# Kernel optimization log

Measured on AMD Instinct MI355X. Metric: run time of the kernel, lower is better.

Reference implementation:

```python
import jax, jax.numpy as jnp
import numpy as np

N_NODES = 50000


def gcn_conv(x, W, b, src, dst, n):
    """PyG-style GCNConv: out = D^-1/2 (A+I) D^-1/2 (x W) + b.
    src/dst: [E] int edge endpoints (messages flow src -> dst)."""
    h = x @ W  # [n, out]
    # degree with self-loops (edge weight 1)
    deg = jax.ops.segment_sum(jnp.ones_like(dst, dtype=h.dtype), dst, num_segments=n) + 1.0
    inv_sqrt = jax.lax.rsqrt(deg)  # [n]
    coef = inv_sqrt[src] * inv_sqrt[dst]  # [E]
    msg = h[src] * coef[:, None]  # [E, out]
    agg = jax.ops.segment_sum(msg, dst, num_segments=n)
    # self-loop contribution: norm = 1/deg
    agg = agg + h * (inv_sqrt * inv_sqrt)[:, None]
    return agg + b


def encoder(x, src, dst, W_a, b_a, W_b, b_b, n):
    h = jax.nn.relu(gcn_conv(x, W_a, b_a, src, dst, n))
    return jax.nn.relu(gcn_conv(h, W_b, b_b, src, dst, n))


def setup_inputs() -> dict:
    key = jax.random.key(0)
    ks = jax.random.split(key, 8)
    N, E = N_NODES, 400000
    d_in, d_hid, d_out = 512, 512, 256
    x = jax.random.normal(ks[0], (N, d_in), dtype=jnp.float32)
    edge_index = jax.random.randint(ks[1], (2, E), 0, N, dtype=jnp.int32)
    edge_index2 = jax.random.randint(ks[2], (2, E), 0, N, dtype=jnp.int32)

    def xavier(k, shape):
        lim = np.sqrt(6.0 / (shape[0] + shape[1]))
        return jax.random.uniform(k, shape, jnp.float32, -lim, lim)

    W1 = xavier(ks[3], (d_in, d_hid))
    b1 = jnp.zeros((d_hid,), jnp.float32)
    W2 = xavier(ks[4], (d_hid, d_out))
    b2 = jnp.zeros((d_out,), jnp.float32)
    W3 = xavier(ks[5], (d_out, d_hid))
    b3 = jnp.zeros((d_hid,), jnp.float32)
    W4 = xavier(ks[6], (d_hid, d_out))
    b4 = jnp.zeros((d_out,), jnp.float32)
    return {"x": x, "edge_index": edge_index, "edge_index2": edge_index2,
            "W1": W1, "b1": b1, "W2": W2, "b2": b2,
            "W3": W3, "b3": b3, "W4": W4, "b4": b4}


def reference(x, edge_index, edge_index2, W1, b1, W2, b2, W3, b3, W4, b4):
    n = x.shape[0]
    z = encoder(x, edge_index[0], edge_index[1], W1, b1, W2, b2, n)
    z_g = encoder(z, edge_index2[0], edge_index2[1], W3, b3, W4, b4, n)
    return (z, z_g)
```

## Files before the change

kernel.cpp:

```cpp
#include <hip/hip_runtime.h>

#define N_NODES 50000
#define MP 50048

typedef short short8 __attribute__((ext_vector_type(8)));
typedef float floatx4 __attribute__((ext_vector_type(4)));
typedef ushort u16x4 __attribute__((ext_vector_type(4)));
typedef float f32x4 __attribute__((ext_vector_type(4)));

__device__ __forceinline__ float bf2f(ushort u) {
    union { unsigned int i; float f; } x; x.i = ((unsigned int)u) << 16; return x.f;
}
__device__ __forceinline__ ushort f2bf(float f) {
    union { float f; unsigned int i; } x; x.f = f;
    unsigned int r = x.i + 0x7FFFu + ((x.i >> 16) & 1u);
    return (ushort)(r >> 16);
}

__global__ __launch_bounds__(256) void deg_int_kernel(const int* __restrict__ dst,
                                                      int* __restrict__ deg, int E) {
    int i = blockIdx.x * 256 + threadIdx.x;
    if (i < E) atomicAdd(&deg[dst[i]], 1);
}
__global__ __launch_bounds__(256) void inv_from_deg(const int* __restrict__ deg,
                                                    float* __restrict__ inv, int n) {
    int i = blockIdx.x * 256 + threadIdx.x;
    if (i < n) inv[i] = rsqrtf((float)deg[i] + 1.0f);
}

__global__ __launch_bounds__(256) void scan1_kernel(const int* __restrict__ deg,
                                                    int* __restrict__ pre,
                                                    int* __restrict__ bsum, int n) {
    __shared__ int tmp[256];
    const int t = threadIdx.x;
    const int i = blockIdx.x * 256 + t;
    const int v = (i < n) ? deg[i] : 0;
    tmp[t] = v;
    __syncthreads();
#pragma unroll
    for (int d = 1; d < 256; d <<= 1) {
        int u = (t >= d) ? tmp[t - d] : 0;
        __syncthreads();
        tmp[t] += u;
        __syncthreads();
    }
    if (i < n) pre[i] = tmp[t] - v;
    if (t == 255) bsum[blockIdx.x] = tmp[255];
}
__global__ __launch_bounds__(256) void scan2_kernel(int* __restrict__ bsum, int nb,
                                                    int* __restrict__ row_ptr_n) {
    __shared__ int tmp[256];
    const int t = threadIdx.x;
    const int v = (t < nb) ? bsum[t] : 0;
    tmp[t] = v;
    __syncthreads();
#pragma unroll
    for (int d = 1; d < 256; d <<= 1) {
        int u = (t >= d) ? tmp[t - d] : 0;
        __syncthreads();
        tmp[t] += u;
        __syncthreads();
    }
    if (t < nb) bsum[t] = tmp[t] - v;
    if (t == 255) *row_ptr_n = tmp[255];
}
__global__ __launch_bounds__(256) void scan3_kernel(const int* __restrict__ pre,
                                                    const int* __restrict__ bsum,
                                                    int* __restrict__ row_ptr,
                                                    int* __restrict__ cursor, int n) {
    const int i = blockIdx.x * 256 + threadIdx.x;
    if (i < n) {
        int v = pre[i] + bsum[blockIdx.x];
        row_ptr[i] = v;
        cursor[i] = v;
    }
}
__global__ __launch_bounds__(256) void fill_adj_kernel(const int* __restrict__ src,
                                                       const int* __restrict__ dst,
                                                       const float* __restrict__ invs,
                                                       int* __restrict__ cursor,
                                                       int* __restrict__ adj,
                                                       float* __restrict__ wgt, int E) {
    int i = blockIdx.x * 256 + threadIdx.x;
    if (i < E) {
        int s = src[i];
        int pos = atomicAdd(&cursor[dst[i]], 1);
        adj[pos] = s;
        wgt[pos] = invs[s];
    }
}

__global__ __launch_bounds__(256) void f2b_kernel(const float* __restrict__ in,
                                                  ushort* __restrict__ out, int n) {
    int i = blockIdx.x * 256 + threadIdx.x;
    if (i < n) out[i] = f2bf(in[i]);
}
__global__ __launch_bounds__(256) void transpose_kernel(const float* __restrict__ W,
                                                        ushort* __restrict__ Wt, int K, int N) {
    int idx = blockIdx.x * 256 + threadIdx.x;
    if (idx < K * N) {
        int k = idx / N, n = idx % N;
        Wt[n * K + k] = f2bf(W[idx]);
    }
}

__global__ __launch_bounds__(512, 4) void gemm_kernel(
    const ushort* __restrict__ A, const ushort* __restrict__ Bt,
    ushort* __restrict__ C, const float* __restrict__ bias,
    int M, int K, int N, int do_relu)
{
    __shared__ __align__(16) ushort Alds[128 * 32];
    __shared__ __align__(16) ushort Blds[128 * 32];
    const int t = threadIdx.x;
    const int w = t >> 6, l = t & 63;
    const int m0 = blockIdx.y * 128;
    const int n0 = blockIdx.x * 128;
    const int wr = (w >> 2) * 64, wc = (w & 3) * 32;
    const int lhi = l >> 4, llo = l & 15;

    floatx4 acc[4][2] = {};

    const int srow = w * 16 + (l >> 2);
    const int scol = (l & 3) * 8;
    int gr = m0 + srow; gr = gr < M ? gr : M - 1;
    const ushort* gA = A + (size_t)gr * K + scol;
    const ushort* gB = Bt + (size_t)(n0 + srow) * K + scol;
    ushort* lA = Alds + srow * 32 + scol;
    ushort* lB = Blds + srow * 32 + scol;

    const int nkt = K >> 5;
    for (int kt = 0; kt < nkt; ++kt) {
        const int k0 = kt << 5;
        __builtin_amdgcn_global_load_lds(
            (const __attribute__((address_space(1))) void*)(gA + k0),
            (__attribute__((address_space(3))) void*)lA, 16, 0, 0);
        __builtin_amdgcn_global_load_lds(
            (const __attribute__((address_space(1))) void*)(gB + k0),
            (__attribute__((address_space(3))) void*)lB, 16, 0, 0);
        __syncthreads();
        short8 av[4], bv[2];
#pragma unroll
        for (int m = 0; m < 4; ++m)
            av[m] = *reinterpret_cast<const short8*>(&Alds[(wr + m * 16 + llo) * 32 + lhi * 8]);
#pragma unroll
        for (int n = 0; n < 2; ++n)
            bv[n] = *reinterpret_cast<const short8*>(&Blds[(wc + n * 16 + llo) * 32 + lhi * 8]);
#pragma unroll
        for (int m = 0; m < 4; ++m)
#pragma unroll
            for (int n = 0; n < 2; ++n)
                acc[m][n] = __builtin_amdgcn_mfma_f32_16x16x32_bf16(av[m], bv[n], acc[m][n], 0, 0, 0);
        __syncthreads();
    }

    const int lr = lhi * 4;
#pragma unroll
    for (int m = 0; m < 4; ++m) {
#pragma unroll
        for (int n = 0; n < 2; ++n) {
            int gcol = n0 + wc + n * 16 + llo;
            float badd = bias ? bias[gcol] : 0.0f;
#pragma unroll
            for (int j = 0; j < 4; ++j) {
                int grow = m0 + wr + m * 16 + lr + j;
                if (grow < M) {
                    float v = acc[m][n][j] + badd;
                    if (do_relu) v = fmaxf(v, 0.0f);
                    C[(size_t)grow * N + gcol] = f2bf(v);
                }
            }
        }
    }
}

template<bool RELU, bool BIAS, bool WF, bool WB>
__global__ __launch_bounds__(256) void gather_kernel(
    const int* __restrict__ row_ptr, const int* __restrict__ adj,
    const float* __restrict__ wgt,
    const ushort* __restrict__ h, int ldh,
    const float* __restrict__ invs, const float* __restrict__ bias,
    float* __restrict__ outF, ushort* __restrict__ outB, int ldo)
{
    const int wv = threadIdx.x >> 6, l = threadIdx.x & 63;
    const int node = blockIdx.x * 4 + wv;
    if (node >= N_NODES) return;
    const int c0 = blockIdx.y * 256 + l * 4;
    const int beg = row_ptr[node], end = row_ptr[node + 1];
    const float invd = invs[node];

    float a0[4] = {0.f, 0.f, 0.f, 0.f}, a1[4] = {0.f, 0.f, 0.f, 0.f};
    int e = beg;
    for (; e + 2 <= end; e += 2) {
        const int s0 = adj[e], s1 = adj[e + 1];
        const float w0 = wgt[e] * invd, w1 = wgt[e + 1] * invd;
        const u16x4 h0 = *reinterpret_cast<const u16x4*>(h + (size_t)s0 * ldh + c0);
        const u16x4 h1 = *reinterpret_cast<const u16x4*>(h + (size_t)s1 * ldh + c0);
#pragma unroll
        for (int k = 0; k < 4; ++k) {
            a0[k] += bf2f(h0[k]) * w0;
            a1[k] += bf2f(h1[k]) * w1;
        }
    }
    if (e < end) {
        const int s0 = adj[e];
        const float w0 = wgt[e] * invd;
        const u16x4 h0 = *reinterpret_cast<const u16x4*>(h + (size_t)s0 * ldh + c0);
#pragma unroll
        for (int k = 0; k < 4; ++k) a0[k] += bf2f(h0[k]) * w0;
    }
    {
        const float ws = invd * invd;
        const u16x4 hs = *reinterpret_cast<const u16x4*>(h + (size_t)node * ldh + c0);
#pragma unroll
        for (int k = 0; k < 4; ++k) a0[k] += a1[k] + bf2f(hs[k]) * ws;
    }
#pragma unroll
    for (int k = 0; k < 4; ++k) {
        float v = a0[k];
        if (BIAS) v += bias[c0 + k];
        if (RELU) v = fmaxf(v, 0.0f);
        a0[k] = v;
    }
    if (WF)
        *reinterpret_cast<f32x4*>(outF + (size_t)node * ldo + c0) = *reinterpret_cast<f32x4*>(a0);
    if (WB) {
        u16x4 o;
#pragma unroll
        for (int k = 0; k < 4; ++k) o[k] = f2bf(a0[k]);
        *reinterpret_cast<u16x4*>(outB + (size_t)node * ldo + c0) = o;
    }
}

extern "C" void kernel_launch(void* const* d_in, const int* in_sizes, int n_in,
                              void* d_out, int out_size, void* d_ws, size_t ws_size,
                              hipStream_t stream)
{
    const float* x  = (const float*)d_in[0];
    const int* ei1  = (const int*)d_in[1];
    const int* ei2  = (const int*)d_in[2];
    const float* W1 = (const float*)d_in[3];
    const float* b1 = (const float*)d_in[4];
    const float* W2 = (const float*)d_in[5];
    const float* b2 = (const float*)d_in[6];
    const float* W3 = (const float*)d_in[7];
    const float* b3 = (const float*)d_in[8];
    const float* W4 = (const float*)d_in[9];
    const float* b4 = (const float*)d_in[10];
    float* z   = (float*)d_out;
    float* z_g = z + (size_t)N_NODES * 256;

    const int E1 = in_sizes[1] / 2, E2 = in_sizes[2] / 2;
    const int* src1 = ei1;  const int* dst1 = ei1 + E1;
    const int* src2 = ei2;  const int* dst2 = ei2 + E2;

    ushort* Xb = (ushort*)z;
    ushort* R1 = (ushort*)z_g;

    char* ws = (char*)d_ws;
    size_t off = 0;
    auto alloc = [&](size_t bytes) { void* p = ws + off; off += (bytes + 255) & ~(size_t)255; return p; };
    ushort* R0   = (ushort*)alloc((size_t)N_NODES * 512 * 2);
    float*  inv1 = (float*) alloc((size_t)N_NODES * 4);
    float*  inv2 = (float*) alloc((size_t)N_NODES * 4);
    int*    deg1 = (int*)   alloc((size_t)N_NODES * 4);
    int*    deg2 = (int*)   alloc((size_t)N_NODES * 4);
    int*    rp1  = (int*)   alloc((size_t)(N_NODES + 1) * 4);
    int*    rp2  = (int*)   alloc((size_t)(N_NODES + 1) * 4);
    int*    cur1 = (int*)   alloc((size_t)N_NODES * 4);
    int*    cur2 = (int*)   alloc((size_t)N_NODES * 4);
    int*    pre1 = (int*)   alloc((size_t)N_NODES * 4);
    int*    pre2 = (int*)   alloc((size_t)N_NODES * 4);
    int*    bs1  = (int*)   alloc(256 * 4);
    int*    bs2  = (int*)   alloc(256 * 4);
    int*    adj1 = (int*)   alloc((size_t)E1 * 4);
    int*    adj2 = (int*)   alloc((size_t)E2 * 4);
    float*  wgt1 = (float*) alloc((size_t)E1 * 4);
    float*  wgt2 = (float*) alloc((size_t)E2 * 4);
    ushort* Wt1  = (ushort*)alloc(512 * 512 * 2);
    ushort* Wt2  = (ushort*)alloc(256 * 512 * 2);
    ushort* Wt3  = (ushort*)alloc(512 * 256 * 2);
    ushort* Wt4  = (ushort*)alloc(256 * 512 * 2);

    const dim3 blk(256);
    const dim3 gblk(512);
    const int MT = MP / 128;
    const int GB = (N_NODES + 3) / 4;
    const int NB = (N_NODES + 255) / 256;

    hipMemsetAsync(deg1, 0, (size_t)N_NODES * 4, stream);
    hipMemsetAsync(deg2, 0, (size_t)N_NODES * 4, stream);
    deg_int_kernel<<<(E1 + 255) / 256, blk, 0, stream>>>(dst1, deg1, E1);
    deg_int_kernel<<<(E2 + 255) / 256, blk, 0, stream>>>(dst2, deg2, E2);
    inv_from_deg<<<(N_NODES + 255) / 256, blk, 0, stream>>>(deg1, inv1, N_NODES);
    inv_from_deg<<<(N_NODES + 255) / 256, blk, 0, stream>>>(deg2, inv2, N_NODES);
    scan1_kernel<<<NB, blk, 0, stream>>>(deg1, pre1, bs1, N_NODES);
    scan1_kernel<<<NB, blk, 0, stream>>>(deg2, pre2, bs2, N_NODES);
    scan2_kernel<<<1, blk, 0, stream>>>(bs1, NB, rp1 + N_NODES);
    scan2_kernel<<<1, blk, 0, stream>>>(bs2, NB, rp2 + N_NODES);
    scan3_kernel<<<NB, blk, 0, stream>>>(pre1, bs1, rp1, cur1, N_NODES);
    scan3_kernel<<<NB, blk, 0, stream>>>(pre2, bs2, rp2, cur2, N_NODES);
    fill_adj_kernel<<<(E1 + 255) / 256, blk, 0, stream>>>(src1, dst1, inv1, cur1, adj1, wgt1, E1);
    fill_adj_kernel<<<(E2 + 255) / 256, blk, 0, stream>>>(src2, dst2, inv2, cur2, adj2, wgt2, E2);

    transpose_kernel<<<(512 * 512 + 255) / 256, blk, 0, stream>>>(W1, Wt1, 512, 512);
    transpose_kernel<<<(512 * 256 + 255) / 256, blk, 0, stream>>>(W2, Wt2, 512, 256);
    transpose_kernel<<<(256 * 512 + 255) / 256, blk, 0, stream>>>(W3, Wt3, 256, 512);
    transpose_kernel<<<(512 * 256 + 255) / 256, blk, 0, stream>>>(W4, Wt4, 512, 256);
    f2b_kernel<<<(N_NODES * 512 + 255) / 256, blk, 0, stream>>>(x, Xb, N_NODES * 512);

    gemm_kernel<<<dim3(4, MT), gblk, 0, stream>>>(Xb, Wt1, R0, nullptr, N_NODES, 512, 512, 0);
    gather_kernel<true, true, false, true><<<dim3(GB, 2), blk, 0, stream>>>(
        rp1, adj1, wgt1, R0, 512, inv1, b1, nullptr, R1, 512);

    gemm_kernel<<<dim3(2, MT), gblk, 0, stream>>>(R1, Wt2, R0, nullptr, N_NODES, 512, 256, 0);
    gather_kernel<true, true, true, true><<<dim3(GB, 1), blk, 0, stream>>>(
        rp1, adj1, wgt1, R0, 256, inv1, b2, z, R1, 256);

    gather_kernel<false, false, false, true><<<dim3(GB, 1), blk, 0, stream>>>(
        rp2, adj2, wgt2, R1, 256, inv2, nullptr, nullptr, R0, 256);
    gemm_kernel<<<dim3(4, MT), gblk, 0, stream>>>(R0, Wt3, R1, b3, N_NODES, 256, 512, 1);

    gemm_kernel<<<dim3(2, MT), gblk, 0, stream>>>(R1, Wt4, R0, nullptr, N_NODES, 512, 256, 0);
    gather_kernel<true, true, true, false><<<dim3(GB, 1), blk, 0, stream>>>(
        rp2, adj2, wgt2, R0, 256, inv2, b4, z_g, nullptr, 256);
}
```

Baseline: 513.6 us.

## Pack adjacency and weights, gather 16-byte rows with two nodes per wavefront

Stores each edge's source index and source normalization weight together as one int2, so each edge needs a single 8-byte load instead of two separate loads. The gather kernel now gives half a wavefront (32 lanes) to each node and has each lane load 8 bf16 values (16 bytes) instead of 4. The edge loop is unrolled by 4 with clamped indices and zero weights for padding edges. This is meant to cut per-edge index traffic and raise memory-level parallelism, at the cost of wasted loads when the two nodes sharing a wavefront have different degrees.

```diff
diff --git a/kernel.cpp b/kernel.cpp
--- a/kernel.cpp
+++ b/kernel.cpp
@@ -5,7 +5,7 @@
 
 typedef short short8 __attribute__((ext_vector_type(8)));
 typedef float floatx4 __attribute__((ext_vector_type(4)));
-typedef ushort u16x4 __attribute__((ext_vector_type(4)));
+typedef ushort u16x8 __attribute__((ext_vector_type(8)));
 typedef float f32x4 __attribute__((ext_vector_type(4)));
 
 __device__ __forceinline__ float bf2f(ushort u) {
@@ -79,14 +79,12 @@
                                                        const int* __restrict__ dst,
                                                        const float* __restrict__ invs,
                                                        int* __restrict__ cursor,
-                                                       int* __restrict__ adj,
-                                                       float* __restrict__ wgt, int E) {
+                                                       int2* __restrict__ adjw, int E) {
     int i = blockIdx.x * 256 + threadIdx.x;
     if (i < E) {
         int s = src[i];
         int pos = atomicAdd(&cursor[dst[i]], 1);
-        adj[pos] = s;
-        wgt[pos] = invs[s];
+        adjw[pos] = make_int2(s, __float_as_int(invs[s]));
     }
 }
 
@@ -175,59 +173,67 @@
 
 template<bool RELU, bool BIAS, bool WF, bool WB>
 __global__ __launch_bounds__(256) void gather_kernel(
-    const int* __restrict__ row_ptr, const int* __restrict__ adj,
-    const float* __restrict__ wgt,
+    const int* __restrict__ row_ptr, const int2* __restrict__ adjw,
     const ushort* __restrict__ h, int ldh,
     const float* __restrict__ invs, const float* __restrict__ bias,
     float* __restrict__ outF, ushort* __restrict__ outB, int ldo)
 {
     const int wv = threadIdx.x >> 6, l = threadIdx.x & 63;
-    const int node = blockIdx.x * 4 + wv;
-    if (node >= N_NODES) return;
-    const int c0 = blockIdx.y * 256 + l * 4;
-    const int beg = row_ptr[node], end = row_ptr[node + 1];
-    const float invd = invs[node];
-
-    float a0[4] = {0.f, 0.f, 0.f, 0.f}, a1[4] = {0.f, 0.f, 0.f, 0.f};
-    int e = beg;
-    for (; e + 2 <= end; e += 2) {
-        const int s0 = adj[e], s1 = adj[e + 1];
-        const float w0 = wgt[e] * invd, w1 = wgt[e + 1] * invd;
-        const u16x4 h0 = *reinterpret_cast<const u16x4*>(h + (size_t)s0 * ldh + c0);
-        const u16x4 h1 = *reinterpret_cast<const u16x4*>(h + (size_t)s1 * ldh + c0);
-#pragma unroll
-        for (int k = 0; k < 4; ++k) {
-            a0[k] += bf2f(h0[k]) * w0;
-            a1[k] += bf2f(h1[k]) * w1;
+    const int half = l >> 5, j = l & 31;
+    const int node = blockIdx.x * 8 + wv * 2 + half;
+    const bool valid = node < N_NODES;
+    const int nd = valid ? node : N_NODES - 1;
+    const int c0 = blockIdx.y * 256 + j * 8;
+    const int beg = row_ptr[nd], end = row_ptr[nd + 1];
+    const float invd = invs[nd];
+    const int deg = end - beg;
+    const int dmax = max(deg, __shfl_xor(deg, 32));
+
+    float a0[8] = {}, a1[8] = {};
+    const int iters = (dmax + 3) >> 2;
+    for (int it = 0; it < iters; ++it) {
+        const int e = beg + it * 4;
+#pragma unroll
+        for (int u = 0; u < 4; ++u) {
+            int ee = e + u;
+            int ec = min(ee, end - 1); ec = max(ec, 0);
+            const int2 aw = adjw[ec];
+            const float w = (ee < end) ? __int_as_float(aw.y) * invd : 0.0f;
+            const u16x8 hv = *reinterpret_cast<const u16x8*>(h + (unsigned)(aw.x * ldh + c0));
+            if (u & 1) {
+#pragma unroll
+                for (int k = 0; k < 8; ++k) a1[k] += bf2f(hv[k]) * w;
+            } else {
+#pragma unroll
+                for (int k = 0; k < 8; ++k) a0[k] += bf2f(hv[k]) * w;
+            }
         }
-    }
-    if (e < end) {
-        const int s0 = adj[e];
-        const float w0 = wgt[e] * invd;
-        const u16x4 h0 = *reinterpret_cast<const u16x4*>(h + (size_t)s0 * ldh + c0);
-#pragma unroll
-        for (int k = 0; k < 4; ++k) a0[k] += bf2f(h0[k]) * w0;
     }
     {
         const float ws = invd * invd;
-        const u16x4 hs = *reinterpret_cast<const u16x4*>(h + (size_t)node * ldh + c0);
-#pragma unroll
-        for (int k = 0; k < 4; ++k) a0[k] += a1[k] + bf2f(hs[k]) * ws;
-    }
-#pragma unroll
-    for (int k = 0; k < 4; ++k) {
+        const u16x8 hs = *reinterpret_cast<const u16x8*>(h + (unsigned)(nd * ldh + c0));
+#pragma unroll
+        for (int k = 0; k < 8; ++k) a0[k] += a1[k] + bf2f(hs[k]) * ws;
+    }
+#pragma unroll
+    for (int k = 0; k < 8; ++k) {
         float v = a0[k];
         if (BIAS) v += bias[c0 + k];
         if (RELU) v = fmaxf(v, 0.0f);
         a0[k] = v;
     }
-    if (WF)
-        *reinterpret_cast<f32x4*>(outF + (size_t)node * ldo + c0) = *reinterpret_cast<f32x4*>(a0);
-    if (WB) {
-        u16x4 o;
-#pragma unroll
-        for (int k = 0; k < 4; ++k) o[k] = f2bf(a0[k]);
-        *reinterpret_cast<u16x4*>(outB + (size_t)node * ldo + c0) = o;
+    if (valid) {
+        if (WF) {
+            float* op = outF + (size_t)node * ldo + c0;
+            *reinterpret_cast<f32x4*>(op)     = *reinterpret_cast<f32x4*>(&a0[0]);
+            *reinterpret_cast<f32x4*>(op + 4) = *reinterpret_cast<f32x4*>(&a0[4]);
+        }
+        if (WB) {
+            u16x8 o;
+#pragma unroll
+            for (int k = 0; k < 8; ++k) o[k] = f2bf(a0[k]);
+            *reinterpret_cast<u16x8*>(outB + (size_t)node * ldo + c0) = o;
+        }
     }
 }
 
@@ -272,10 +278,8 @@
     int*    pre2 = (int*)   alloc((size_t)N_NODES * 4);
     int*    bs1  = (int*)   alloc(256 * 4);
     int*    bs2  = (int*)   alloc(256 * 4);
-    int*    adj1 = (int*)   alloc((size_t)E1 * 4);
-    int*    adj2 = (int*)   alloc((size_t)E2 * 4);
-    float*  wgt1 = (float*) alloc((size_t)E1 * 4);
-    float*  wgt2 = (float*) alloc((size_t)E2 * 4);
+    int2*   adjw1= (int2*)  alloc((size_t)E1 * 8);
+    int2*   adjw2= (int2*)  alloc((size_t)E2 * 8);
     ushort* Wt1  = (ushort*)alloc(512 * 512 * 2);
     ushort* Wt2  = (ushort*)alloc(256 * 512 * 2);
     ushort* Wt3  = (ushort*)alloc(512 * 256 * 2);
@@ -284,7 +288,7 @@
     const dim3 blk(256);
     const dim3 gblk(512);
     const int MT = MP / 128;
-    const int GB = (N_NODES + 3) / 4;
+    const int GB = (N_NODES + 7) / 8;
     const int NB = (N_NODES + 255) / 256;
 
     hipMemsetAsync(deg1, 0, (size_t)N_NODES * 4, stream);
@@ -299,8 +303,8 @@
     scan2_kernel<<<1, blk, 0, stream>>>(bs2, NB, rp2 + N_NODES);
     scan3_kernel<<<NB, blk, 0, stream>>>(pre1, bs1, rp1, cur1, N_NODES);
     scan3_kernel<<<NB, blk, 0, stream>>>(pre2, bs2, rp2, cur2, N_NODES);
-    fill_adj_kernel<<<(E1 + 255) / 256, blk, 0, stream>>>(src1, dst1, inv1, cur1, adj1, wgt1, E1);
-    fill_adj_kernel<<<(E2 + 255) / 256, blk, 0, stream>>>(src2, dst2, inv2, cur2, adj2, wgt2, E2);
+    fill_adj_kernel<<<(E1 + 255) / 256, blk, 0, stream>>>(src1, dst1, inv1, cur1, adjw1, E1);
+    fill_adj_kernel<<<(E2 + 255) / 256, blk, 0, stream>>>(src2, dst2, inv2, cur2, adjw2, E2);
 
     transpose_kernel<<<(512 * 512 + 255) / 256, blk, 0, stream>>>(W1, Wt1, 512, 512);
     transpose_kernel<<<(512 * 256 + 255) / 256, blk, 0, stream>>>(W2, Wt2, 512, 256);
@@ -310,17 +314,17 @@
 
     gemm_kernel<<<dim3(4, MT), gblk, 0, stream>>>(Xb, Wt1, R0, nullptr, N_NODES, 512, 512, 0);
     gather_kernel<true, true, false, true><<<dim3(GB, 2), blk, 0, stream>>>(
-        rp1, adj1, wgt1, R0, 512, inv1, b1, nullptr, R1, 512);
+        rp1, adjw1, R0, 512, inv1, b1, nullptr, R1, 512);
 
     gemm_kernel<<<dim3(2, MT), gblk, 0, stream>>>(R1, Wt2, R0, nullptr, N_NODES, 512, 256, 0);
     gather_kernel<true, true, true, true><<<dim3(GB, 1), blk, 0, stream>>>(
-        rp1, adj1, wgt1, R0, 256, inv1, b2, z, R1, 256);
+        rp1, adjw1, R0, 256, inv1, b2, z, R1, 256);
 
     gather_kernel<false, false, false, true><<<dim3(GB, 1), blk, 0, stream>>>(
-        rp2, adj2, wgt2, R1, 256, inv2, nullptr, nullptr, R0, 256);
+        rp2, adjw2, R1, 256, inv2, nullptr, nullptr, R0, 256);
     gemm_kernel<<<dim3(4, MT), gblk, 0, stream>>>(R0, Wt3, R1, b3, N_NODES, 256, 512, 1);
 
     gemm_kernel<<<dim3(2, MT), gblk, 0, stream>>>(R1, Wt4, R0, nullptr, N_NODES, 512, 256, 0);
     gather_kernel<true, true, true, false><<<dim3(GB, 1), blk, 0, stream>>>(
-        rp2, adj2, wgt2, R0, 256, inv2, b4, z_g, nullptr, 256);
-}
+        rp2, adjw2, R0, 256, inv2, b4, z_g, nullptr, 256);
+}
```

New measurement: 503.2 us. 2.0% less time.

## Fuse fp32-to-bf16 input cast into first GEMM and widen gather kernels

Applied to the files above, without the earlier changes.

Drops the separate f2b pass over x and converts fp32 rows to bf16 while staging into LDS inside a new GEMM variant, so the 100MB fp32 input is read only once. Packs each edge's source index and weight into one int2 array. Adds a 512-wide gather that handles a full row per wave with 8-element loads instead of two grid-y halves. Unrolls all gathers to 4 edges with four accumulators and uses 32-bit index arithmetic. The new A path uses ordinary register loads rather than global_load_lds, and the unchanged row-clamping leaves tail handling as before.

```diff
diff --git a/kernel.cpp b/kernel.cpp
--- a/kernel.cpp
+++ b/kernel.cpp
@@ -6,6 +6,7 @@
 typedef short short8 __attribute__((ext_vector_type(8)));
 typedef float floatx4 __attribute__((ext_vector_type(4)));
 typedef ushort u16x4 __attribute__((ext_vector_type(4)));
+typedef ushort u16x8 __attribute__((ext_vector_type(8)));
 typedef float f32x4 __attribute__((ext_vector_type(4)));
 
 __device__ __forceinline__ float bf2f(ushort u) {
@@ -79,22 +80,15 @@
                                                        const int* __restrict__ dst,
                                                        const float* __restrict__ invs,
                                                        int* __restrict__ cursor,
-                                                       int* __restrict__ adj,
-                                                       float* __restrict__ wgt, int E) {
+                                                       int2* __restrict__ adjw, int E) {
     int i = blockIdx.x * 256 + threadIdx.x;
     if (i < E) {
         int s = src[i];
         int pos = atomicAdd(&cursor[dst[i]], 1);
-        adj[pos] = s;
-        wgt[pos] = invs[s];
-    }
-}
-
-__global__ __launch_bounds__(256) void f2b_kernel(const float* __restrict__ in,
-                                                  ushort* __restrict__ out, int n) {
-    int i = blockIdx.x * 256 + threadIdx.x;
-    if (i < n) out[i] = f2bf(in[i]);
-}
+        adjw[pos] = make_int2(s, __float_as_int(invs[s]));
+    }
+}
+
 __global__ __launch_bounds__(256) void transpose_kernel(const float* __restrict__ W,
                                                         ushort* __restrict__ Wt, int K, int N) {
     int idx = blockIdx.x * 256 + threadIdx.x;
@@ -173,10 +167,139 @@
     }
 }
 
+__global__ __launch_bounds__(512, 4) void gemm_f32a_kernel(
+    const float* __restrict__ A, const ushort* __restrict__ Bt,
+    ushort* __restrict__ C, int M, int K, int N)
+{
+    __shared__ __align__(16) ushort Alds[128 * 32];
+    __shared__ __align__(16) ushort Blds[128 * 32];
+    const int t = threadIdx.x;
+    const int w = t >> 6, l = t & 63;
+    const int m0 = blockIdx.y * 128;
+    const int n0 = blockIdx.x * 128;
+    const int wr = (w >> 2) * 64, wc = (w & 3) * 32;
+    const int lhi = l >> 4, llo = l & 15;
+
+    floatx4 acc[4][2] = {};
+
+    const int srow = w * 16 + (l >> 2);
+    const int scol = (l & 3) * 8;
+    int gr = m0 + srow; gr = gr < M ? gr : M - 1;
+    const float*  gA = A + (size_t)gr * K + scol;
+    const ushort* gB = Bt + (size_t)(n0 + srow) * K + scol;
+    ushort* lA = Alds + srow * 32 + scol;
+    ushort* lB = Blds + srow * 32 + scol;
+
+    const int nkt = K >> 5;
+    for (int kt = 0; kt < nkt; ++kt) {
+        const int k0 = kt << 5;
+        __builtin_amdgcn_global_load_lds(
+            (const __attribute__((address_space(1))) void*)(gB + k0),
+            (__attribute__((address_space(3))) void*)lB, 16, 0, 0);
+        const f32x4 alo = *reinterpret_cast<const f32x4*>(gA + k0);
+        const f32x4 ahi = *reinterpret_cast<const f32x4*>(gA + k0 + 4);
+        u16x8 ab;
+#pragma unroll
+        for (int k = 0; k < 4; ++k) { ab[k] = f2bf(alo[k]); ab[k + 4] = f2bf(ahi[k]); }
+        *reinterpret_cast<u16x8*>(lA) = ab;
+        __syncthreads();
+        short8 av[4], bv[2];
+#pragma unroll
+        for (int m = 0; m < 4; ++m)
+            av[m] = *reinterpret_cast<const short8*>(&Alds[(wr + m * 16 + llo) * 32 + lhi * 8]);
+#pragma unroll
+        for (int n = 0; n < 2; ++n)
+            bv[n] = *reinterpret_cast<const short8*>(&Blds[(wc + n * 16 + llo) * 32 + lhi * 8]);
+#pragma unroll
+        for (int m = 0; m < 4; ++m)
+#pragma unroll
+            for (int n = 0; n < 2; ++n)
+                acc[m][n] = __builtin_amdgcn_mfma_f32_16x16x32_bf16(av[m], bv[n], acc[m][n], 0, 0, 0);
+        __syncthreads();
+    }
+
+    const int lr = lhi * 4;
+#pragma unroll
+    for (int m = 0; m < 4; ++m) {
+#pragma unroll
+        for (int n = 0; n < 2; ++n) {
+            int gcol = n0 + wc + n * 16 + llo;
+#pragma unroll
+            for (int j = 0; j < 4; ++j) {
+                int grow = m0 + wr + m * 16 + lr + j;
+                if (grow < M)
+                    C[(size_t)grow * N + gcol] = f2bf(acc[m][n][j]);
+            }
+        }
+    }
+}
+
+__global__ __launch_bounds__(256) void gather512_kernel(
+    const int* __restrict__ row_ptr, const int2* __restrict__ adjw,
+    const ushort* __restrict__ h, const float* __restrict__ invs,
+    const float* __restrict__ bias, ushort* __restrict__ outB)
+{
+    const int wv = threadIdx.x >> 6, l = threadIdx.x & 63;
+    const int node = blockIdx.x * 4 + wv;
+    if (node >= N_NODES) return;
+    const int c0 = l * 8;
+    const int beg = row_ptr[node], end = row_ptr[node + 1];
+    const float invd = invs[node];
+
+    float a0[8] = {}, a1[8] = {}, a2[8] = {}, a3[8] = {};
+    int e = beg;
+    for (; e + 4 <= end; e += 4) {
+        const int2 w0 = adjw[e], w1 = adjw[e+1], w2 = adjw[e+2], w3 = adjw[e+3];
+        const float f0 = __int_as_float(w0.y) * invd, f1 = __int_as_float(w1.y) * invd;
+        const float f2 = __int_as_float(w2.y) * invd, f3 = __int_as_float(w3.y) * invd;
+        const u16x8 h0 = *reinterpret_cast<const u16x8*>(h + (unsigned)(w0.x * 512 + c0));
+        const u16x8 h1 = *reinterpret_cast<const u16x8*>(h + (unsigned)(w1.x * 512 + c0));
+        const u16x8 h2 = *reinterpret_cast<const u16x8*>(h + (unsigned)(w2.x * 512 + c0));
+        const u16x8 h3 = *reinterpret_cast<const u16x8*>(h + (unsigned)(w3.x * 512 + c0));
+#pragma unroll
+        for (int k = 0; k < 8; ++k) {
+            a0[k] += bf2f(h0[k]) * f0;
+            a1[k] += bf2f(h1[k]) * f1;
+            a2[k] += bf2f(h2[k]) * f2;
+            a3[k] += bf2f(h3[k]) * f3;
+        }
+    }
+    if (e + 2 <= end) {
+        const int2 w0 = adjw[e], w1 = adjw[e+1];
+        const float f0 = __int_as_float(w0.y) * invd, f1 = __int_as_float(w1.y) * invd;
+        const u16x8 h0 = *reinterpret_cast<const u16x8*>(h + (unsigned)(w0.x * 512 + c0));
+        const u16x8 h1 = *reinterpret_cast<const u16x8*>(h + (unsigned)(w1.x * 512 + c0));
+#pragma unroll
+        for (int k = 0; k < 8; ++k) {
+            a0[k] += bf2f(h0[k]) * f0;
+            a1[k] += bf2f(h1[k]) * f1;
+        }
+        e += 2;
+    }
+    if (e < end) {
+        const int2 w0 = adjw[e];
+        const float f0 = __int_as_float(w0.y) * invd;
+        const u16x8 h0 = *reinterpret_cast<const u16x8*>(h + (unsigned)(w0.x * 512 + c0));
+#pragma unroll
+        for (int k = 0; k < 8; ++k) a0[k] += bf2f(h0[k]) * f0;
+    }
+    {
+        const float ws = invd * invd;
+        const u16x8 hs = *reinterpret_cast<const u16x8*>(h + (unsigned)(node * 512 + c0));
+#pragma unroll
+        for (int k = 0; k < 8; ++k)
+            a0[k] = (a0[k] + a1[k]) + (a2[k] + a3[k]) + bf2f(hs[k]) * ws;
+    }
+    u16x8 o;
+#pragma unroll
+    for (int k = 0; k < 8; ++k)
+        o[k] = f2bf(fmaxf(a0[k] + bias[c0 + k], 0.0f));
+    *reinterpret_cast<u16x8*>(outB + (size_t)node * 512 + c0) = o;
+}
+
 template<bool RELU, bool BIAS, bool WF, bool WB>
 __global__ __launch_bounds__(256) void gather_kernel(
-    const int* __restrict__ row_ptr, const int* __restrict__ adj,
-    const float* __restrict__ wgt,
+    const int* __restrict__ row_ptr, const int2* __restrict__ adjw,
     const ushort* __restrict__ h, int ldh,
     const float* __restrict__ invs, const float* __restrict__ bias,
     float* __restrict__ outF, ushort* __restrict__ outB, int ldo)
@@ -184,35 +307,53 @@
     const int wv = threadIdx.x >> 6, l = threadIdx.x & 63;
     const int node = blockIdx.x * 4 + wv;
     if (node >= N_NODES) return;
-    const int c0 = blockIdx.y * 256 + l * 4;
+    const int c0 = l * 4;
     const int beg = row_ptr[node], end = row_ptr[node + 1];
     const float invd = invs[node];
 
-    float a0[4] = {0.f, 0.f, 0.f, 0.f}, a1[4] = {0.f, 0.f, 0.f, 0.f};
+    float a0[4] = {}, a1[4] = {}, a2[4] = {}, a3[4] = {};
     int e = beg;
-    for (; e + 2 <= end; e += 2) {
-        const int s0 = adj[e], s1 = adj[e + 1];
-        const float w0 = wgt[e] * invd, w1 = wgt[e + 1] * invd;
-        const u16x4 h0 = *reinterpret_cast<const u16x4*>(h + (size_t)s0 * ldh + c0);
-        const u16x4 h1 = *reinterpret_cast<const u16x4*>(h + (size_t)s1 * ldh + c0);
+    for (; e + 4 <= end; e += 4) {
+        const int2 w0 = adjw[e], w1 = adjw[e+1], w2 = adjw[e+2], w3 = adjw[e+3];
+        const float f0 = __int_as_float(w0.y) * invd, f1 = __int_as_float(w1.y) * invd;
+        const float f2 = __int_as_float(w2.y) * invd, f3 = __int_as_float(w3.y) * invd;
+        const u16x4 h0 = *reinterpret_cast<const u16x4*>(h + (unsigned)(w0.x * ldh + c0));
+        const u16x4 h1 = *reinterpret_cast<const u16x4*>(h + (unsigned)(w1.x * ldh + c0));
+        const u16x4 h2 = *reinterpret_cast<const u16x4*>(h + (unsigned)(w2.x * ldh + c0));
+        const u16x4 h3 = *reinterpret_cast<const u16x4*>(h + (unsigned)(w3.x * ldh + c0));
 #pragma unroll
         for (int k = 0; k < 4; ++k) {
-            a0[k] += bf2f(h0[k]) * w0;
-            a1[k] += bf2f(h1[k]) * w1;
-        }
+            a0[k] += bf2f(h0[k]) * f0;
+            a1[k] += bf2f(h1[k]) * f1;
+            a2[k] += bf2f(h2[k]) * f2;
+            a3[k] += bf2f(h3[k]) * f3;
+        }
+    }
+    if (e + 2 <= end) {
+        const int2 w0 = adjw[e], w1 = adjw[e+1];
+        const float f0 = __int_as_float(w0.y) * invd, f1 = __int_as_float(w1.y) * invd;
+        const u16x4 h0 = *reinterpret_cast<const u16x4*>(h + (unsigned)(w0.x * ldh + c0));
+        const u16x4 h1 = *reinterpret_cast<const u16x4*>(h + (unsigned)(w1.x * ldh + c0));
+#pragma unroll
+        for (int k = 0; k < 4; ++k) {
+            a0[k] += bf2f(h0[k]) * f0;
+            a1[k] += bf2f(h1[k]) * f1;
+        }
+        e += 2;
     }
     if (e < end) {
-        const int s0 = adj[e];
-        const float w0 = wgt[e] * invd;
-        const u16x4 h0 = *reinterpret_cast<const u16x4*>(h + (size_t)s0 * ldh + c0);
-#pragma unroll
-        for (int k = 0; k < 4; ++k) a0[k] += bf2f(h0[k]) * w0;
+        const int2 w0 = adjw[e];
+        const float f0 = __int_as_float(w0.y) * invd;
+        const u16x4 h0 = *reinterpret_cast<const u16x4*>(h + (unsigned)(w0.x * ldh + c0));
+#pragma unroll
+        for (int k = 0; k < 4; ++k) a0[k] += bf2f(h0[k]) * f0;
     }
     {
         const float ws = invd * invd;
-        const u16x4 hs = *reinterpret_cast<const u16x4*>(h + (size_t)node * ldh + c0);
-#pragma unroll
-        for (int k = 0; k < 4; ++k) a0[k] += a1[k] + bf2f(hs[k]) * ws;
+        const u16x4 hs = *reinterpret_cast<const u16x4*>(h + (unsigned)(node * ldh + c0));
+#pragma unroll
+        for (int k = 0; k < 4; ++k)
+            a0[k] = (a0[k] + a1[k]) + (a2[k] + a3[k]) + bf2f(hs[k]) * ws;
     }
 #pragma unroll
     for (int k = 0; k < 4; ++k) {
@@ -253,7 +394,6 @@
     const int* src1 = ei1;  const int* dst1 = ei1 + E1;
     const int* src2 = ei2;  const int* dst2 = ei2 + E2;
 
-    ushort* Xb = (ushort*)z;
     ushort* R1 = (ushort*)z_g;
 
     char* ws = (char*)d_ws;
@@ -272,10 +412,8 @@
     int*    pre2 = (int*)   alloc((size_t)N_NODES * 4);
     int*    bs1  = (int*)   alloc(256 * 4);
     int*    bs2  = (int*)   alloc(256 * 4);
-    int*    adj1 = (int*)   alloc((size_t)E1 * 4);
-    int*    adj2 = (int*)   alloc((size_t)E2 * 4);
-    float*  wgt1 = (float*) alloc((size_t)E1 * 4);
-    float*  wgt2 = (float*) alloc((size_t)E2 * 4);
+    int2*   adjw1= (int2*)  alloc((size_t)E1 * 8);
+    int2*   adjw2= (int2*)  alloc((size_t)E2 * 8);
     ushort* Wt1  = (ushort*)alloc(512 * 512 * 2);
     ushort* Wt2  = (ushort*)alloc(256 * 512 * 2);
     ushort* Wt3  = (ushort*)alloc(512 * 256 * 2);
@@ -299,28 +437,26 @@
     scan2_kernel<<<1, blk, 0, stream>>>(bs2, NB, rp2 + N_NODES);
     scan3_kernel<<<NB, blk, 0, stream>>>(pre1, bs1, rp1, cur1, N_NODES);
     scan3_kernel<<<NB, blk, 0, stream>>>(pre2, bs2, rp2, cur2, N_NODES);
-    fill_adj_kernel<<<(E1 + 255) / 256, blk, 0, stream>>>(src1, dst1, inv1, cur1, adj1, wgt1, E1);
-    fill_adj_kernel<<<(E2 + 255) / 256, blk, 0, stream>>>(src2, dst2, inv2, cur2, adj2, wgt2, E2);
+    fill_adj_kernel<<<(E1 + 255) / 256, blk, 0, stream>>>(src1, dst1, inv1, cur1, adjw1, E1);
+    fill_adj_kernel<<<(E2 + 255) / 256, blk, 0, stream>>>(src2, dst2, inv2, cur2, adjw2, E2);
 
     transpose_kernel<<<(512 * 512 + 255) / 256, blk, 0, stream>>>(W1, Wt1, 512, 512);
     transpose_kernel<<<(512 * 256 + 255) / 256, blk, 0, stream>>>(W2, Wt2, 512, 256);
     transpose_kernel<<<(256 * 512 + 255) / 256, blk, 0, stream>>>(W3, Wt3, 256, 512);
     transpose_kernel<<<(512 * 256 + 255) / 256, blk, 0, stream>>>(W4, Wt4, 512, 256);
-    f2b_kernel<<<(N_NODES * 512 + 255) / 256, blk, 0, stream>>>(x, Xb, N_NODES * 512);
-
-    gemm_kernel<<<dim3(4, MT), gblk, 0, stream>>>(Xb, Wt1, R0, nullptr, N_NODES, 512, 512, 0);
-    gather_kernel<true, true, false, true><<<dim3(GB, 2), blk, 0, stream>>>(
-        rp1, adj1, wgt1, R0, 512, inv1, b1, nullptr, R1, 512);
+
+    gemm_f32a_kernel<<<dim3(4, MT), gblk, 0, stream>>>(x, Wt1, R0, N_NODES, 512, 512);
+    gather512_kernel<<<GB, blk, 0, stream>>>(rp1, adjw1, R0, inv1, b1, R1);
 
     gemm_kernel<<<dim3(2, MT), gblk, 0, stream>>>(R1, Wt2, R0, nullptr, N_NODES, 512, 256, 0);
-    gather_kernel<true, true, true, true><<<dim3(GB, 1), blk, 0, stream>>>(
-        rp1, adj1, wgt1, R0, 256, inv1, b2, z, R1, 256);
-
-    gather_kernel<false, false, false, true><<<dim3(GB, 1), blk, 0, stream>>>(
-        rp2, adj2, wgt2, R1, 256, inv2, nullptr, nullptr, R0, 256);
+    gather_kernel<true, true, true, true><<<GB, blk, 0, stream>>>(
+        rp1, adjw1, R0, 256, inv1, b2, z, R1, 256);
+
+    gather_kernel<false, false, false, true><<<GB, blk, 0, stream>>>(
+        rp2, adjw2, R1, 256, inv2, nullptr, nullptr, R0, 256);
     gemm_kernel<<<dim3(4, MT), gblk, 0, stream>>>(R0, Wt3, R1, b3, N_NODES, 256, 512, 1);
 
     gemm_kernel<<<dim3(2, MT), gblk, 0, stream>>>(R1, Wt4, R0, nullptr, N_NODES, 512, 256, 0);
-    gather_kernel<true, true, true, false><<<dim3(GB, 1), blk, 0, stream>>>(
-        rp2, adj2, wgt2, R0, 256, inv2, b4, z_g, nullptr, 256);
-}
+    gather_kernel<true, true, true, false><<<GB, blk, 0, stream>>>(
+        rp2, adjw2, R0, 256, inv2, b4, z_g, nullptr, 256);
+}
```

After: 471.0 us. -8.3%, faster.
